# Kernel optimization log

Measured on AMD Instinct MI355X. Metric: run time of the kernel, lower is better.

The kernel has to match this reference:

```python
import jax, jax.numpy as jnp
import numpy as np

V, E, D, OUT = 100000, 400000, 128, 128
KP = 20  # kron projection dim (hard-coded 20 in module; 20*20=400)
EPS = 1e-5


def _layer_norm(x, g, b):
    mu = jnp.mean(x, axis=-1, keepdims=True)
    var = jnp.mean(jnp.square(x - mu), axis=-1, keepdims=True)
    return (x - mu) * jax.lax.rsqrt(var + EPS) * g + b


def setup_inputs() -> dict:
    key = jax.random.key(0)
    ks = jax.random.split(key, 16)
    def lin(k, fan_in, shape):
        return jax.random.normal(k, shape, jnp.float32) / np.sqrt(fan_in)
    inp = {
        'node_feats': jax.random.normal(ks[0], (V, D), jnp.float32),
        'src': jax.random.randint(ks[1], (E,), 0, V, jnp.int32),
        'dst': jax.random.randint(ks[2], (E,), 0, V, jnp.int32),
        # project_edge: Linear(2D, 1)
        'W_edge': lin(ks[3], 2 * D, (2 * D, 1)), 'b_edge': jnp.zeros((1,), jnp.float32),
        # attentive_gru.project_node: Linear(D, D)
        'W_pn': lin(ks[4], D, (D, D)), 'b_pn': jnp.zeros((D,), jnp.float32),
        # GRUCell(D, D)
        'W_ih': lin(ks[5], D, (3 * D, D)), 'b_ih': jnp.zeros((3 * D,), jnp.float32),
        'W_hh': lin(ks[6], D, (3 * D, D)), 'b_hh': jnp.zeros((3 * D,), jnp.float32),
        # layer_norm(D)
        'ln_g': jnp.ones((D,), jnp.float32), 'ln_b': jnp.zeros((D,), jnp.float32),
        # kron.proj_node: Linear(D, 20)+LN
        'Wk1': lin(ks[7], D, (D, KP)), 'bk1': jnp.zeros((KP,), jnp.float32),
        'lnk1_g': jnp.ones((KP,), jnp.float32), 'lnk1_b': jnp.zeros((KP,), jnp.float32),
        # kron.proj_kron: Linear(400, OUT)+LN
        'Wk2': lin(ks[8], KP * KP, (KP * KP, OUT)), 'bk2': jnp.zeros((OUT,), jnp.float32),
        'lnk2_g': jnp.ones((OUT,), jnp.float32), 'lnk2_b': jnp.zeros((OUT,), jnp.float32),
        # concat_proj: Linear(D+OUT, D)+LN
        'Wc': lin(ks[9], D + OUT, (D + OUT, D)), 'bc': jnp.zeros((D,), jnp.float32),
        'lnc_g': jnp.ones((D,), jnp.float32), 'lnc_b': jnp.zeros((D,), jnp.float32),
    }
    return inp


def _forward(node_feats, W_edge, b_edge, W_pn, b_pn, W_ih, b_ih, W_hh, b_hh,
             ln_g, ln_b, Wk1, bk1, lnk1_g, lnk1_b, Wk2, bk2, lnk2_g, lnk2_b,
             Wc, bc, lnc_g, lnc_b, src, dst):
    n = node_feats.shape[0]
    d = node_feats.shape[1]
    # --- Kronecker message branch ---
    npj = jax.nn.relu(_layer_norm(node_feats @ Wk1 + bk1, lnk1_g, lnk1_b))  # [V,20]
    kron = (npj[src][:, :, None] * npj[dst][:, None, :]).reshape(src.shape[0], -1)  # [E,400]
    kron = jax.nn.relu(_layer_norm(kron @ Wk2 + bk2, lnk2_g, lnk2_b))  # [E,OUT]
    kron_feat = jax.ops.segment_sum(kron, dst, num_segments=n)  # [V,OUT]
    # --- Attention branch: he = cat(dst_feats, src_feats) ---
    he = jnp.concatenate([node_feats[dst], node_feats[src]], axis=1)  # [E,2D]
    logits = jax.nn.relu(he @ W_edge + b_edge)  # [E,1]
    # edge softmax over in-edges of each dst node
    lmax = jax.ops.segment_max(logits, dst, num_segments=n)  # [V,1]
    a = jnp.exp(logits - lmax[dst])
    asum = jax.ops.segment_sum(a, dst, num_segments=n)
    a = a / asum[dst]  # [E,1]
    hv = node_feats @ W_pn + b_pn  # [V,D]
    context = jax.nn.relu(jax.ops.segment_sum(hv[src] * a, dst, num_segments=n))  # [V,D]
    # --- GRUCell(context, node_feats) ---
    gi = context @ W_ih.T + b_ih
    gh = node_feats @ W_hh.T + b_hh
    r = jax.nn.sigmoid(gi[:, :d] + gh[:, :d])
    z = jax.nn.sigmoid(gi[:, d:2 * d] + gh[:, d:2 * d])
    nn_ = jnp.tanh(gi[:, 2 * d:] + r * gh[:, 2 * d:])
    h = (1.0 - z) * nn_ + z * node_feats
    gru_out = _layer_norm(jax.nn.relu(h), ln_g, ln_b)  # [V,D]
    # --- concat + projection ---
    cat = jnp.concatenate([gru_out, kron_feat], axis=1)  # [V,D+OUT]
    return jax.nn.relu(_layer_norm(cat @ Wc + bc, lnc_g, lnc_b))


def reference(node_feats, src, dst, W_edge, b_edge, W_pn, b_pn, W_ih, b_ih, W_hh, b_hh,
              ln_g, ln_b, Wk1, bk1, lnk1_g, lnk1_b, Wk2, bk2, lnk2_g, lnk2_b,
              Wc, bc, lnc_g, lnc_b):
    return _forward(node_feats, W_edge, b_edge, W_pn, b_pn, W_ih, b_ih, W_hh, b_hh,
                    ln_g, ln_b, Wk1, bk1, lnk1_g, lnk1_b, Wk2, bk2, lnk2_g, lnk2_b,
                    Wc, bc, lnc_g, lnc_b, src, dst)
```

## Files before the change

kernel.cpp:

```cpp
#include <hip/hip_runtime.h>

#define G_KP 20
#define G_LN_EPS 1e-5f

typedef float v4f __attribute__((ext_vector_type(4)));
typedef short v8s __attribute__((ext_vector_type(8)));
typedef short v4s __attribute__((ext_vector_type(4)));

__device__ __forceinline__ unsigned short f2b(float x) {
  union { float f; unsigned int i; } c;
  c.f = x;
  return (unsigned short)((c.i + 0x7FFFu + ((c.i >> 16) & 1u)) >> 16);
}
__device__ __forceinline__ float b2f(unsigned short u) {
  union { unsigned int i; float f; } c;
  c.i = ((unsigned int)u) << 16;
  return c.f;
}

template<int NKT, int NT>
__device__ __forceinline__ void stage_mfma(
    const v8s* __restrict__ Bsrc, int kt_tiles, v8s* B_lds,
    const unsigned short* Arow, int a_kt, int a_off,
    int t, int l, v4f* acc) {
  constexpr int NPR = NT / 4;
  v8s pr[NPR];
  #pragma unroll
  for (int i = 0; i < NPR; ++i) pr[i] = Bsrc[t + i * 256];
  #pragma unroll
  for (int kt = 0; kt < NKT; ++kt) {
    __syncthreads();
    #pragma unroll
    for (int i = 0; i < NPR; ++i) B_lds[t + i * 256] = pr[i];
    if (kt + 1 < NKT) {
      #pragma unroll
      for (int i = 0; i < NPR; ++i)
        pr[i] = Bsrc[(kt + 1) * kt_tiles * 64 + t + i * 256];
    }
    __syncthreads();
    v8s a = *(const v8s*)&Arow[kt * a_kt + a_off];
    #pragma unroll
    for (int n0 = 0; n0 < NT; ++n0)
      acc[n0] = __builtin_amdgcn_mfma_f32_16x16x32_bf16(a, B_lds[n0 * 64 + l], acc[n0], 0, 0, 0);
  }
}

__global__ void GNNLayerKAFP_76871324663923_kernel() {}

__global__ void k_fill(float* out, int n, float v) {
  int i = blockIdx.x * 256 + threadIdx.x;
  if (i < n) out[i] = v;
}

__global__ void k_zero(float* p, int n) {
  int i = blockIdx.x * 256 + threadIdx.x;
  if (i < n) p[i] = 0.0f;
}

__global__ void k_prep_wk2b(const float* Wk2, unsigned short* Wk2b) {
  int id = blockIdx.x * 256 + threadIdx.x;
  if (id >= 13 * 8 * 64 * 8) return;
  int j = id & 7, l = (id >> 3) & 63, n0 = (id >> 9) & 7, kt = id >> 12;
  int k = kt * 32 + (l >> 4) * 8 + j;
  int n = n0 * 16 + (l & 15);
  Wk2b[id] = f2b((k < 400) ? Wk2[k * 128 + n] : 0.0f);
}

__global__ void k_prep_wpnb(const float* Wpn, unsigned short* WpnB) {
  int id = blockIdx.x * 256 + threadIdx.x;
  if (id >= 4 * 8 * 64 * 8) return;
  int j = id & 7, l = (id >> 3) & 63, n0 = (id >> 9) & 7, kt = id >> 12;
  int k = kt * 32 + (l >> 4) * 8 + j;
  int n = n0 * 16 + (l & 15);
  WpnB[id] = f2b(Wpn[k * 128 + n]);
}

__global__ void k_prep_wgb(const float* Wih, const float* Whh, unsigned short* WgB) {
  int id = blockIdx.x * 256 + threadIdx.x;
  if (id >= 8 * 32 * 64 * 8) return;
  int j = id & 7, l = (id >> 3) & 63, n0 = (id >> 9) & 31, kt = id >> 14;
  int k = kt * 32 + (l >> 4) * 8 + j;
  int jj = n0 * 16 + (l & 15);
  float v = 0.0f;
  if (jj < 256)      v = (k < 128) ? Wih[jj * 128 + k] : Whh[jj * 128 + (k - 128)];
  else if (jj < 384) { if (k < 128)  v = Wih[jj * 128 + k]; }
  else               { if (k >= 128) v = Whh[(jj - 128) * 128 + (k - 128)]; }
  WgB[id] = f2b(v);
}

__global__ void k_prep_wcb(const float* Wc, unsigned short* WcB) {
  int id = blockIdx.x * 256 + threadIdx.x;
  if (id >= 8 * 8 * 64 * 8) return;
  int j = id & 7, l = (id >> 3) & 63, n0 = (id >> 9) & 7, kt = id >> 12;
  int k = kt * 32 + (l >> 4) * 8 + j;
  int n = n0 * 16 + (l & 15);
  WcB[id] = f2b(Wc[k * 128 + n]);
}

__global__ void k_npj(const float* nf, const float* Wk1, const float* bk1,
                      const float* g, const float* b, float* npj) {
  int v = blockIdx.x;
  int lane = threadIdx.x;
  __shared__ float x[128];
  __shared__ float y[G_KP];
  __shared__ float st[2];
  x[lane]      = nf[v * 128 + lane];
  x[lane + 64] = nf[v * 128 + 64 + lane];
  __syncthreads();
  if (lane < G_KP) {
    float acc = bk1[lane];
    for (int t = 0; t < 128; ++t) acc += x[t] * Wk1[t * G_KP + lane];
    y[lane] = acc;
  }
  __syncthreads();
  if (lane == 0) {
    float s = 0.0f, ss = 0.0f;
    for (int i = 0; i < G_KP; ++i) { s += y[i]; ss += y[i] * y[i]; }
    float mu = s * (1.0f / G_KP);
    float var = ss * (1.0f / G_KP) - mu * mu;
    st[0] = mu;
    st[1] = rsqrtf(fmaxf(var, 0.0f) + G_LN_EPS);
  }
  __syncthreads();
  if (lane < G_KP) {
    float val = (y[lane] - st[0]) * st[1] * g[lane] + b[lane];
    npj[v * G_KP + lane] = fmaxf(val, 0.0f);
  }
}

__global__ void k_pdps(const float* nf, const float* We, float* pd, float* ps,
                       int nV) {
  int w = threadIdx.x >> 6, l = threadIdx.x & 63;
  int v = blockIdx.x * 4 + w;
  if (v >= nV) return;
  float x0 = nf[v * 128 + l], x1 = nf[v * 128 + 64 + l];
  float p0 = x0 * We[l]       + x1 * We[64 + l];
  float p1 = x0 * We[128 + l] + x1 * We[192 + l];
  for (int off = 32; off > 0; off >>= 1) {
    p0 += __shfl_down(p0, off, 64);
    p1 += __shfl_down(p1, off, 64);
  }
  if (l == 0) { pd[v] = p0; ps[v] = p1; }
}

__global__ void k_hist(const int* dst, int* deg, int nE) {
  int e = blockIdx.x * 256 + threadIdx.x;
  if (e < nE) atomicAdd(&deg[dst[e]], 1);
}

__global__ void k_scan1(const int* deg, int* bsum, int nV) {
  __shared__ int red[256];
  int b = blockIdx.x, t = threadIdx.x;
  int base = b * 2048 + t * 8;
  int s = 0;
  #pragma unroll
  for (int k = 0; k < 8; ++k) {
    int i = base + k;
    if (i < nV) s += deg[i];
  }
  red[t] = s;
  __syncthreads();
  for (int off = 128; off > 0; off >>= 1) {
    if (t < off) red[t] += red[t + off];
    __syncthreads();
  }
  if (t == 0) bsum[b] = red[0];
}

__global__ void k_scan2(const int* bsum, int* boff, int* total, int nB) {
  __shared__ int sh[1024];
  int t = threadIdx.x;
  int v = (t < nB) ? bsum[t] : 0;
  sh[t] = v;
  __syncthreads();
  for (int off = 1; off < 1024; off <<= 1) {
    int u = (t >= off) ? sh[t - off] : 0;
    __syncthreads();
    sh[t] += u;
    __syncthreads();
  }
  if (t < nB) boff[t] = sh[t] - v;
  if (t == 1023) total[0] = sh[1023];
}

__global__ void k_scan3(const int* deg, const int* boff, const int* total,
                        int* rowptr, int* cursor, int nV) {
  __shared__ int sh[256];
  int b = blockIdx.x, t = threadIdx.x;
  int base = b * 2048 + t * 8;
  int loc[8];
  int s = 0;
  #pragma unroll
  for (int k = 0; k < 8; ++k) {
    int i = base + k;
    int d = (i < nV) ? deg[i] : 0;
    loc[k] = s; s += d;
  }
  sh[t] = s;
  __syncthreads();
  for (int off = 1; off < 256; off <<= 1) {
    int u = (t >= off) ? sh[t - off] : 0;
    __syncthreads();
    sh[t] += u;
    __syncthreads();
  }
  int toff = sh[t] - s + boff[b];
  #pragma unroll
  for (int k = 0; k < 8; ++k) {
    int i = base + k;
    if (i < nV) { rowptr[i] = toff + loc[k]; cursor[i] = toff + loc[k]; }
  }
  if (b == 0 && t == 0) rowptr[nV] = total[0];
}

__global__ void k_edge(const int* src, const int* dst, const float* pd,
                       const float* ps, const float* be, float* a,
                       int* cursor, int* eid, int nE) {
  int e = blockIdx.x * 256 + threadIdx.x;
  if (e >= nE) return;
  int d = dst[e], s_ = src[e];
  float lg = fmaxf(pd[d] + ps[s_] + be[0], 0.0f);
  a[e] = __expf(fminf(lg, 60.0f));
  int pos = atomicAdd(&cursor[d], 1);
  eid[pos] = e;
}

__global__ void k_ctx_gather(const int* rowptr, const int* eid, const int* src,
                             const float* a, const float* nf, float* wctx,
                             int nV) {
  int w = threadIdx.x >> 6, l = threadIdx.x & 63;
  int v = blockIdx.x * 4 + w;
  if (v >= nV) return;
  int beg = rowptr[v], end = rowptr[v + 1];
  float s = 0.0f;
  for (int i = beg; i < end; ++i) s += a[eid[i]];
  float dn = 1.0f / fmaxf(s, 1e-20f);
  float a0 = 0.0f, a1 = 0.0f;
  for (int i = beg; i < end; ++i) {
    int e = eid[i];
    float c = a[e] * dn;
    int sn = src[e];
    a0 += c * nf[sn * 128 + l];
    a1 += c * nf[sn * 128 + 64 + l];
  }
  wctx[v * 128 + l]      = a0;
  wctx[v * 128 + 64 + l] = a1;
}

__global__ void __launch_bounds__(256, 2)
k_kron_mfma(const int* src, const int* dst, const float* npj,
            const int* rowptr, const int* eid,
            const unsigned short* Wk2b, const float* bk2,
            const float* g, const float* b, float* kf, int nE) {
  __shared__ unsigned short A_lds[64 * 424];
  __shared__ int eidx[64][2];
  __shared__ unsigned short SDB[4096];
  unsigned short (*sd)[40] = (unsigned short(*)[40])SDB;
  v8s* B_lds = (v8s*)SDB;
  float* Yf = (float*)A_lds;

  int t = threadIdx.x;
  int w = t >> 6, l = t & 63;
  int c15 = l & 15, quad = l >> 4;
  int ebase4 = w * 16;

  int ebeg = blockIdx.x * 64;
  int ecnt = nE - ebeg; if (ecnt > 64) ecnt = 64;

  if (l < 16) {
    int i = ebase4 + l;
    int e = eid[(i < ecnt) ? (ebeg + i) : ebeg];
    eidx[i][0] = src[e];
    eidx[i][1] = dst[e];
  }
  #pragma unroll
  for (int k = 0; k < 10; ++k) {
    int i = l + k * 64;
    int er = i / 40, p = i - er * 40;
    int e = ebase4 + er;
    float v = (p < 20) ? npj[eidx[e][0] * G_KP + p]
                       : npj[eidx[e][1] * G_KP + (p - 20)];
    sd[e][p] = f2b(v);
  }
  #pragma unroll
  for (int k = 0; k < 4; ++k) {
    int i = l + k * 64;
    int e = ebase4 + (i >> 4), kk = 400 + (i & 15);
    A_lds[e * 424 + kk] = 0;
  }
  #pragma unroll
  for (int k = 0; k < 5; ++k) {
    int task = l + k * 64;
    int er = task / 20;
    int i20 = task - er * 20;
    int e = ebase4 + er;
    float s = b2f(sd[e][i20]);
    int base = e * 424 + i20 * 20;
    #pragma unroll
    for (int j20 = 0; j20 < 20; ++j20)
      A_lds[base + j20] = f2b(s * b2f(sd[e][20 + j20]));
  }

  v4f acc[8];
  #pragma unroll
  for (int n0 = 0; n0 < 8; ++n0)
    #pragma unroll
    for (int r = 0; r < 4; ++r) acc[n0][r] = 0.0f;

  stage_mfma<13, 8>((const v8s*)Wk2b, 8, B_lds,
                    &A_lds[(ebase4 + c15) * 424], 32, quad * 8, t, l, acc);

  float biasv[8], gv[8], bv[8];
  #pragma unroll
  for (int n0 = 0; n0 < 8; ++n0) {
    int n = n0 * 16 + c15;
    biasv[n0] = bk2[n]; gv[n0] = g[n]; bv[n0] = b[n];
  }
  float mu[4], rs[4];
  #pragma unroll
  for (int r = 0; r < 4; ++r) {
    float s = 0.0f, q = 0.0f;
    #pragma unroll
    for (int n0 = 0; n0 < 8; ++n0) {
      float v = acc[n0][r] + biasv[n0];
      s += v; q += v * v;
    }
    for (int m = 1; m < 16; m <<= 1) {
      s += __shfl_xor(s, m, 64);
      q += __shfl_xor(q, m, 64);
    }
    float mm = s * (1.0f / 128.0f);
    float vv = q * (1.0f / 128.0f) - mm * mm;
    mu[r] = mm;
    rs[r] = rsqrtf(fmaxf(vv, 0.0f) + G_LN_EPS);
  }
  __syncthreads();
  #pragma unroll
  for (int r = 0; r < 4; ++r) {
    int eloc = ebase4 + quad * 4 + r;
    #pragma unroll
    for (int n0 = 0; n0 < 8; ++n0) {
      float v = acc[n0][r] + biasv[n0];
      Yf[eloc * 132 + n0 * 16 + c15] =
          fmaxf((v - mu[r]) * rs[r] * gv[n0] + bv[n0], 0.0f);
    }
  }
  __syncthreads();

  int dF = eidx[0][1];
  int dL = eidx[ecnt - 1][1];
  int col = t & 127;
  int wend = ebeg + ecnt;
  for (int d = dF + (t >> 7); d <= dL; d += 2) {
    int rb = rowptr[d], re = rowptr[d + 1];
    int lo = (rb > ebeg ? rb : ebeg) - ebeg;
    int hi = (re < wend ? re : wend) - ebeg;
    if (lo >= hi) continue;
    float s = 0.0f;
    for (int i = lo; i < hi; ++i) s += Yf[i * 132 + col];
    if (rb >= ebeg && re <= wend)
      kf[(size_t)d * 128 + col] = s;
    else
      atomicAdd(&kf[(size_t)d * 128 + col], s);
  }
}

__global__ void __launch_bounds__(256, 2)
k_gru_mfma(const float* nf, const float* wctx, const float* kf,
           const unsigned short* WpnB, const float* bpn,
           const unsigned short* WgB,
           const float* b_ih, const float* b_hh,
           const float* g1, const float* b1,
           const unsigned short* WcB, const float* bc,
           const float* g2, const float* b2, float* out,
           int nV) {
  __shared__ unsigned short CX[64][264];
  __shared__ v8s B_lds[1024];
  int t = threadIdx.x;
  int w = t >> 6, l = t & 63;
  int c15 = l & 15, quad = l >> 4;
  int v0 = blockIdx.x * 64;
  int rowbase = w * 16;

  #pragma unroll
  for (int k = 0; k < 8; ++k) {
    int i = l + k * 64;
    int r = i >> 5;
    int seg = i & 31;
    int vn = v0 + rowbase + r; if (vn >= nV) vn = nV - 1;
    v4f wc = *(const v4f*)&wctx[vn * 128 + seg * 4];
    v4f xf = *(const v4f*)&nf[vn * 128 + seg * 4];
    v4s pw = { (short)f2b(wc[0]), (short)f2b(wc[1]), (short)f2b(wc[2]), (short)f2b(wc[3]) };
    v4s px = { (short)f2b(xf[0]), (short)f2b(xf[1]), (short)f2b(xf[2]), (short)f2b(xf[3]) };
    *(v4s*)&CX[rowbase + r][seg * 4]       = pw;
    *(v4s*)&CX[rowbase + r][128 + seg * 4] = px;
  }

  {
    v4f acc[8];
    #pragma unroll
    for (int n0 = 0; n0 < 8; ++n0)
      #pragma unroll
      for (int r = 0; r < 4; ++r) acc[n0][r] = 0.0f;
    stage_mfma<4, 8>((const v8s*)WpnB, 8, B_lds,
                     &CX[rowbase + c15][0], 32, quad * 8, t, l, acc);
    #pragma unroll
    for (int n0 = 0; n0 < 8; ++n0) {
      int n = n0 * 16 + c15;
      float bo = bpn[n];
      #pragma unroll
      for (int r = 0; r < 4; ++r)
        CX[rowbase + quad * 4 + r][n] = f2b(fmaxf(acc[n0][r] + bo, 0.0f));
    }
  }

  unsigned int rz[32];
  {
    v4f acc[16];
    #pragma unroll
    for (int n0 = 0; n0 < 16; ++n0)
      #pragma unroll
      for (int r = 0; r < 4; ++r) acc[n0][r] = 0.0f;
    stage_mfma<8, 16>((const v8s*)WgB, 32, B_lds,
                      &CX[rowbase + c15][0], 32, quad * 8, t, l, acc);
    #pragma unroll
    for (int n0 = 0; n0 < 8; ++n0) {
      int j = n0 * 16 + c15;
      float brz = b_ih[j] + b_hh[j];
      float bzz = b_ih[128 + j] + b_hh[128 + j];
      #pragma unroll
      for (int r = 0; r < 4; ++r) {
        float rp = acc[n0][r] + brz;
        float zp = acc[8 + n0][r] + bzz;
        float rr = 1.0f / (1.0f + __expf(-fmaxf(fminf(rp, 30.0f), -30.0f)));
        float zz = 1.0f / (1.0f + __expf(-fmaxf(fminf(zp, 30.0f), -30.0f)));
        rz[r * 8 + n0] = (unsigned int)f2b(rr) | ((unsigned int)f2b(zz) << 16);
      }
    }
  }
  {
    v4f acc[16];
    #pragma unroll
    for (int n0 = 0; n0 < 16; ++n0)
      #pragma unroll
      for (int r = 0; r < 4; ++r) acc[n0][r] = 0.0f;
    stage_mfma<8, 16>((const v8s*)WgB + 16 * 64, 32, B_lds,
                      &CX[rowbase + c15][0], 32, quad * 8, t, l, acc);
    #pragma unroll
    for (int r = 0; r < 4; ++r) {
      int row = rowbase + quad * 4 + r;
      float h[8];
      float s = 0.0f, q = 0.0f;
      #pragma unroll
      for (int n0 = 0; n0 < 8; ++n0) {
        int j = n0 * 16 + c15;
        float gi = acc[n0][r] + b_ih[256 + j];
        float gh = acc[8 + n0][r] + b_hh[256 + j];
        unsigned int pk = rz[r * 8 + n0];
        float rr = b2f((unsigned short)(pk & 0xFFFFu));
        float zz = b2f((unsigned short)(pk >> 16));
        float an = fmaxf(fminf(gi + rr * gh, 15.0f), -15.0f);
        float e2 = __expf(-2.0f * an);
        float nn = (1.0f - e2) / (1.0f + e2);
        float x  = b2f(CX[row][128 + j]);
        float hv = fmaxf((1.0f - zz) * nn + zz * x, 0.0f);
        h[n0] = hv; s += hv; q += hv * hv;
      }
      for (int m = 1; m < 16; m <<= 1) {
        s += __shfl_xor(s, m, 64);
        q += __shfl_xor(q, m, 64);
      }
      float mu = s * (1.0f / 128.0f);
      float var = q * (1.0f / 128.0f) - mu * mu;
      float rstd = rsqrtf(fmaxf(var, 0.0f) + G_LN_EPS);
      #pragma unroll
      for (int n0 = 0; n0 < 8; ++n0) {
        int j = n0 * 16 + c15;
        CX[row][j] = f2b((h[n0] - mu) * rstd * g1[j] + b1[j]);
      }
    }
  }

  #pragma unroll
  for (int k = 0; k < 8; ++k) {
    int i = l + k * 64;
    int r = i >> 5, seg = i & 31;
    int vn = v0 + rowbase + r; if (vn >= nV) vn = nV - 1;
    v4f kv = *(const v4f*)&kf[vn * 128 + seg * 4];
    v4s pk = { (short)f2b(kv[0]), (short)f2b(kv[1]), (short)f2b(kv[2]), (short)f2b(kv[3]) };
    *(v4s*)&CX[rowbase + r][128 + seg * 4] = pk;
  }

  {
    v4f acc[8];
    #pragma unroll
    for (int n0 = 0; n0 < 8; ++n0)
      #pragma unroll
      for (int r = 0; r < 4; ++r) acc[n0][r] = 0.0f;
    stage_mfma<8, 8>((const v8s*)WcB, 8, B_lds,
                     &CX[rowbase + c15][0], 32, quad * 8, t, l, acc);
    #pragma unroll
    for (int r = 0; r < 4; ++r) {
      float vv[8];
      float s = 0.0f, q = 0.0f;
      #pragma unroll
      for (int n0 = 0; n0 < 8; ++n0) {
        vv[n0] = acc[n0][r] + bc[n0 * 16 + c15];
        s += vv[n0]; q += vv[n0] * vv[n0];
      }
      for (int m = 1; m < 16; m <<= 1) {
        s += __shfl_xor(s, m, 64);
        q += __shfl_xor(q, m, 64);
      }
      float mu = s * (1.0f / 128.0f);
      float var = q * (1.0f / 128.0f) - mu * mu;
      float rstd = rsqrtf(fmaxf(var, 0.0f) + G_LN_EPS);
      int vn = v0 + rowbase + quad * 4 + r;
      if (vn < nV) {
        #pragma unroll
        for (int n0 = 0; n0 < 8; ++n0) {
          int n = n0 * 16 + c15;
          float y = fmaxf((vv[n0] - mu) * rstd * g2[n] + b2[n], 0.0f);
          if (y != y) y = 9.0f;
          out[vn * 128 + n] = y;
        }
      }
    }
  }
}

extern "C" void kernel_launch(void* const* d_in, const int* in_sizes, int n_in,
                              void* d_out, int out_size, void* d_ws, size_t ws_size,
                              hipStream_t stream) {
  (void)n_in;

  int nV = in_sizes[0] / 128;
  int nE = in_sizes[1];

  const float* nf     = (const float*)d_in[0];
  const int*   src    = (const int*)d_in[1];
  const int*   dst    = (const int*)d_in[2];
  const float* W_edge = (const float*)d_in[3];
  const float* b_edge = (const float*)d_in[4];
  const float* W_pn   = (const float*)d_in[5];
  const float* b_pn   = (const float*)d_in[6];
  const float* W_ih   = (const float*)d_in[7];
  const float* b_ih   = (const float*)d_in[8];
  const float* W_hh   = (const float*)d_in[9];
  const float* b_hh   = (const float*)d_in[10];
  const float* ln_g   = (const float*)d_in[11];
  const float* ln_b   = (const float*)d_in[12];
  const float* Wk1    = (const float*)d_in[13];
  const float* bk1    = (const float*)d_in[14];
  const float* lnk1_g = (const float*)d_in[15];
  const float* lnk1_b = (const float*)d_in[16];
  const float* Wk2    = (const float*)d_in[17];
  const float* bk2    = (const float*)d_in[18];
  const float* lnk2_g = (const float*)d_in[19];
  const float* lnk2_b = (const float*)d_in[20];
  const float* Wc     = (const float*)d_in[21];
  const float* bc     = (const float*)d_in[22];
  const float* lnc_g  = (const float*)d_in[23];
  const float* lnc_b  = (const float*)d_in[24];

  float* ws = (float*)d_ws;
  size_t off = 0;
  float* w_npj  = ws + off; off += (size_t)nV * G_KP;
  float* w_a    = ws + off; off += (size_t)nE;
  float* w_pd   = ws + off; off += (size_t)nV;
  float* w_ps   = ws + off; off += (size_t)nV;
  int*   w_rowp = (int*)(ws + off); off += (size_t)nV + 1;
  int*   w_curs = (int*)(ws + off); off += (size_t)nV;
  int*   w_eid  = (int*)(ws + off); off += (size_t)nE;
  int*   w_bsum = (int*)(ws + off); off += 1024;
  int*   w_boff = (int*)(ws + off); off += 1024;
  int*   w_tot  = (int*)(ws + off); off += 1;
  float* w_wctx = ws + off; off += (size_t)nV * 128;
  int*   w_deg  = (int*)(ws + off); off += (size_t)nV;
  float* w_kf   = ws + off; off += (size_t)nV * 128;
  unsigned short* w_wk2b = (unsigned short*)(ws + off); off += 26624;
  unsigned short* w_wpnb = (unsigned short*)(ws + off); off += 8192;
  unsigned short* w_wgb  = (unsigned short*)(ws + off); off += 65536;
  unsigned short* w_wcb  = (unsigned short*)(ws + off); off += 16384;
  size_t need_bytes = off * 4;

  if (ws_size < need_bytes) {
    k_fill<<<(out_size + 255) / 256, 256, 0, stream>>>((float*)d_out, out_size, 7.0f);
    return;
  }

  k_fill<<<(out_size + 255) / 256, 256, 0, stream>>>((float*)d_out, out_size, 2.0f);

  int nzero = nV * 129;
  k_zero<<<(nzero + 255) / 256, 256, 0, stream>>>((float*)w_deg, nzero);
  k_prep_wk2b<<<208, 256, 0, stream>>>(Wk2, w_wk2b);
  k_prep_wpnb<<<64, 256, 0, stream>>>(W_pn, w_wpnb);
  k_prep_wgb<<<512, 256, 0, stream>>>(W_ih, W_hh, w_wgb);
  k_prep_wcb<<<128, 256, 0, stream>>>(Wc, w_wcb);

  int nB = (nV + 2047) / 2048;
  k_npj<<<nV, 64, 0, stream>>>(nf, Wk1, bk1, lnk1_g, lnk1_b, w_npj);
  k_pdps<<<(nV + 3) / 4, 256, 0, stream>>>(nf, W_edge, w_pd, w_ps, nV);
  k_hist<<<(nE + 255) / 256, 256, 0, stream>>>(dst, w_deg, nE);
  k_scan1<<<nB, 256, 0, stream>>>(w_deg, w_bsum, nV);
  k_scan2<<<1, 1024, 0, stream>>>(w_bsum, w_boff, w_tot, nB);
  k_scan3<<<nB, 256, 0, stream>>>(w_deg, w_boff, w_tot, w_rowp, w_curs, nV);
  k_edge<<<(nE + 255) / 256, 256, 0, stream>>>(src, dst, w_pd, w_ps, b_edge,
                                               w_a, w_curs, w_eid, nE);
  k_ctx_gather<<<(nV + 3) / 4, 256, 0, stream>>>(w_rowp, w_eid, src, w_a, nf,
                                                 w_wctx, nV);
  k_kron_mfma<<<(nE + 63) / 64, 256, 0, stream>>>(src, dst, w_npj, w_rowp,
                                                  w_eid, w_wk2b, bk2,
                                                  lnk2_g, lnk2_b, w_kf, nE);
  k_gru_mfma<<<(nV + 63) / 64, 256, 0, stream>>>(nf, w_wctx, w_kf, w_wpnb, b_pn,
                                                 w_wgb, b_ih, b_hh, ln_g, ln_b,
                                                 w_wcb, bc, lnc_g, lnc_b,
                                                 (float*)d_out, nV);
}
```

Before: 770.1 us.

## Split kron MFMA work across wave pairs with 32-edge blocks

The kron kernel now handles 32 edges per block instead of 64. Each pair of waves shares a 16-edge row tile, and each wave computes half of the 128 output columns. LayerNorm statistics are combined across the two halves through a small shared-memory exchange, and launch bounds are raised to allow more resident blocks. The aim is less LDS and fewer registers per block for higher occupancy, at the cost of twice as many blocks, extra barriers, and more reloading of the B weights and boundary segment-sum work.

```diff
diff --git a/kernel.cpp b/kernel.cpp
--- a/kernel.cpp
+++ b/kernel.cpp
@@ -18,12 +18,12 @@
   return c.f;
 }
 
-template<int NKT, int NT>
-__device__ __forceinline__ void stage_mfma(
+template<int NKT, int NTS, int NTU>
+__device__ __forceinline__ void stage_mfma2(
     const v8s* __restrict__ Bsrc, int kt_tiles, v8s* B_lds,
-    const unsigned short* Arow, int a_kt, int a_off,
+    const unsigned short* Arow, int a_kt, int a_off, int b_off,
     int t, int l, v4f* acc) {
-  constexpr int NPR = NT / 4;
+  constexpr int NPR = NTS / 4;
   v8s pr[NPR];
   #pragma unroll
   for (int i = 0; i < NPR; ++i) pr[i] = Bsrc[t + i * 256];
@@ -40,8 +40,8 @@
     __syncthreads();
     v8s a = *(const v8s*)&Arow[kt * a_kt + a_off];
     #pragma unroll
-    for (int n0 = 0; n0 < NT; ++n0)
-      acc[n0] = __builtin_amdgcn_mfma_f32_16x16x32_bf16(a, B_lds[n0 * 64 + l], acc[n0], 0, 0, 0);
+    for (int n0 = 0; n0 < NTU; ++n0)
+      acc[n0] = __builtin_amdgcn_mfma_f32_16x16x32_bf16(a, B_lds[b_off + n0 * 64 + l], acc[n0], 0, 0, 0);
   }
 }
 
@@ -247,14 +247,15 @@
   wctx[v * 128 + 64 + l] = a1;
 }
 
-__global__ void __launch_bounds__(256, 2)
+__global__ void __launch_bounds__(256, 4)
 k_kron_mfma(const int* src, const int* dst, const float* npj,
             const int* rowptr, const int* eid,
             const unsigned short* Wk2b, const float* bk2,
             const float* g, const float* b, float* kf, int nE) {
-  __shared__ unsigned short A_lds[64 * 424];
-  __shared__ int eidx[64][2];
+  __shared__ unsigned short A_lds[32 * 424];
+  __shared__ int eidx[32][2];
   __shared__ unsigned short SDB[4096];
+  __shared__ float psq[2][2][16][2];
   unsigned short (*sd)[40] = (unsigned short(*)[40])SDB;
   v8s* B_lds = (v8s*)SDB;
   float* Yf = (float*)A_lds;
@@ -262,66 +263,60 @@
   int t = threadIdx.x;
   int w = t >> 6, l = t & 63;
   int c15 = l & 15, quad = l >> 4;
-  int ebase4 = w * 16;
-
-  int ebeg = blockIdx.x * 64;
-  int ecnt = nE - ebeg; if (ecnt > 64) ecnt = 64;
-
-  if (l < 16) {
-    int i = ebase4 + l;
-    int e = eid[(i < ecnt) ? (ebeg + i) : ebeg];
-    eidx[i][0] = src[e];
-    eidx[i][1] = dst[e];
-  }
-  #pragma unroll
-  for (int k = 0; k < 10; ++k) {
-    int i = l + k * 64;
+  int pg = w >> 1, hf = w & 1;
+  int erbase = pg * 16;
+
+  int ebeg = blockIdx.x * 32;
+  int ecnt = nE - ebeg; if (ecnt > 32) ecnt = 32;
+
+  if (t < 32) {
+    int e = eid[(t < ecnt) ? (ebeg + t) : ebeg];
+    eidx[t][0] = src[e];
+    eidx[t][1] = dst[e];
+  }
+  __syncthreads();
+  for (int i = t; i < 1280; i += 256) {
     int er = i / 40, p = i - er * 40;
-    int e = ebase4 + er;
-    float v = (p < 20) ? npj[eidx[e][0] * G_KP + p]
-                       : npj[eidx[e][1] * G_KP + (p - 20)];
-    sd[e][p] = f2b(v);
-  }
-  #pragma unroll
-  for (int k = 0; k < 4; ++k) {
-    int i = l + k * 64;
-    int e = ebase4 + (i >> 4), kk = 400 + (i & 15);
+    float v = (p < 20) ? npj[eidx[er][0] * G_KP + p]
+                       : npj[eidx[er][1] * G_KP + (p - 20)];
+    sd[er][p] = f2b(v);
+  }
+  __syncthreads();
+  for (int i = t; i < 32 * 16; i += 256) {
+    int e = i >> 4, kk = 400 + (i & 15);
     A_lds[e * 424 + kk] = 0;
   }
-  #pragma unroll
-  for (int k = 0; k < 5; ++k) {
-    int task = l + k * 64;
-    int er = task / 20;
-    int i20 = task - er * 20;
-    int e = ebase4 + er;
-    float s = b2f(sd[e][i20]);
-    int base = e * 424 + i20 * 20;
+  for (int task = t; task < 640; task += 256) {
+    int er = task / 20, i20 = task - er * 20;
+    float s = b2f(sd[er][i20]);
+    int base = er * 424 + i20 * 20;
     #pragma unroll
     for (int j20 = 0; j20 < 20; ++j20)
-      A_lds[base + j20] = f2b(s * b2f(sd[e][20 + j20]));
-  }
-
-  v4f acc[8];
-  #pragma unroll
-  for (int n0 = 0; n0 < 8; ++n0)
+      A_lds[base + j20] = f2b(s * b2f(sd[er][20 + j20]));
+  }
+
+  v4f acc[4];
+  #pragma unroll
+  for (int n0 = 0; n0 < 4; ++n0)
     #pragma unroll
     for (int r = 0; r < 4; ++r) acc[n0][r] = 0.0f;
 
-  stage_mfma<13, 8>((const v8s*)Wk2b, 8, B_lds,
-                    &A_lds[(ebase4 + c15) * 424], 32, quad * 8, t, l, acc);
-
-  float biasv[8], gv[8], bv[8];
-  #pragma unroll
-  for (int n0 = 0; n0 < 8; ++n0) {
-    int n = n0 * 16 + c15;
+  stage_mfma2<13, 8, 4>((const v8s*)Wk2b, 8, B_lds,
+                        &A_lds[(erbase + c15) * 424], 32, quad * 8,
+                        hf * 256, t, l, acc);
+
+  float biasv[4], gv[4], bv[4];
+  #pragma unroll
+  for (int n0 = 0; n0 < 4; ++n0) {
+    int n = hf * 64 + n0 * 16 + c15;
     biasv[n0] = bk2[n]; gv[n0] = g[n]; bv[n0] = b[n];
   }
-  float mu[4], rs[4];
+  float sArr[4], qArr[4];
   #pragma unroll
   for (int r = 0; r < 4; ++r) {
     float s = 0.0f, q = 0.0f;
     #pragma unroll
-    for (int n0 = 0; n0 < 8; ++n0) {
+    for (int n0 = 0; n0 < 4; ++n0) {
       float v = acc[n0][r] + biasv[n0];
       s += v; q += v * v;
     }
@@ -329,19 +324,30 @@
       s += __shfl_xor(s, m, 64);
       q += __shfl_xor(q, m, 64);
     }
+    sArr[r] = s; qArr[r] = q;
+    if (c15 == 0) {
+      psq[pg][hf][quad * 4 + r][0] = s;
+      psq[pg][hf][quad * 4 + r][1] = q;
+    }
+  }
+  __syncthreads();
+  float mu[4], rs[4];
+  #pragma unroll
+  for (int r = 0; r < 4; ++r) {
+    float s = sArr[r] + psq[pg][hf ^ 1][quad * 4 + r][0];
+    float q = qArr[r] + psq[pg][hf ^ 1][quad * 4 + r][1];
     float mm = s * (1.0f / 128.0f);
     float vv = q * (1.0f / 128.0f) - mm * mm;
     mu[r] = mm;
     rs[r] = rsqrtf(fmaxf(vv, 0.0f) + G_LN_EPS);
   }
-  __syncthreads();
   #pragma unroll
   for (int r = 0; r < 4; ++r) {
-    int eloc = ebase4 + quad * 4 + r;
-    #pragma unroll
-    for (int n0 = 0; n0 < 8; ++n0) {
+    int eloc = erbase + quad * 4 + r;
+    #pragma unroll
+    for (int n0 = 0; n0 < 4; ++n0) {
       float v = acc[n0][r] + biasv[n0];
-      Yf[eloc * 132 + n0 * 16 + c15] =
+      Yf[eloc * 132 + hf * 64 + n0 * 16 + c15] =
           fmaxf((v - mu[r]) * rs[r] * gv[n0] + bv[n0], 0.0f);
     }
   }
@@ -402,8 +408,8 @@
     for (int n0 = 0; n0 < 8; ++n0)
       #pragma unroll
       for (int r = 0; r < 4; ++r) acc[n0][r] = 0.0f;
-    stage_mfma<4, 8>((const v8s*)WpnB, 8, B_lds,
-                     &CX[rowbase + c15][0], 32, quad * 8, t, l, acc);
+    stage_mfma2<4, 8, 8>((const v8s*)WpnB, 8, B_lds,
+                         &CX[rowbase + c15][0], 32, quad * 8, 0, t, l, acc);
     #pragma unroll
     for (int n0 = 0; n0 < 8; ++n0) {
       int n = n0 * 16 + c15;
@@ -421,8 +427,8 @@
     for (int n0 = 0; n0 < 16; ++n0)
       #pragma unroll
       for (int r = 0; r < 4; ++r) acc[n0][r] = 0.0f;
-    stage_mfma<8, 16>((const v8s*)WgB, 32, B_lds,
-                      &CX[rowbase + c15][0], 32, quad * 8, t, l, acc);
+    stage_mfma2<8, 16, 16>((const v8s*)WgB, 32, B_lds,
+                           &CX[rowbase + c15][0], 32, quad * 8, 0, t, l, acc);
     #pragma unroll
     for (int n0 = 0; n0 < 8; ++n0) {
       int j = n0 * 16 + c15;
@@ -444,8 +450,8 @@
     for (int n0 = 0; n0 < 16; ++n0)
       #pragma unroll
       for (int r = 0; r < 4; ++r) acc[n0][r] = 0.0f;
-    stage_mfma<8, 16>((const v8s*)WgB + 16 * 64, 32, B_lds,
-                      &CX[rowbase + c15][0], 32, quad * 8, t, l, acc);
+    stage_mfma2<8, 16, 16>((const v8s*)WgB + 16 * 64, 32, B_lds,
+                           &CX[rowbase + c15][0], 32, quad * 8, 0, t, l, acc);
     #pragma unroll
     for (int r = 0; r < 4; ++r) {
       int row = rowbase + quad * 4 + r;
@@ -497,8 +503,8 @@
     for (int n0 = 0; n0 < 8; ++n0)
       #pragma unroll
       for (int r = 0; r < 4; ++r) acc[n0][r] = 0.0f;
-    stage_mfma<8, 8>((const v8s*)WcB, 8, B_lds,
-                     &CX[rowbase + c15][0], 32, quad * 8, t, l, acc);
+    stage_mfma2<8, 8, 8>((const v8s*)WcB, 8, B_lds,
+                         &CX[rowbase + c15][0], 32, quad * 8, 0, t, l, acc);
     #pragma unroll
     for (int r = 0; r < 4; ++r) {
       float vv[8];
@@ -609,7 +615,7 @@
                                                w_a, w_curs, w_eid, nE);
   k_ctx_gather<<<(nV + 3) / 4, 256, 0, stream>>>(w_rowp, w_eid, src, w_a, nf,
                                                  w_wctx, nV);
-  k_kron_mfma<<<(nE + 63) / 64, 256, 0, stream>>>(src, dst, w_npj, w_rowp,
+  k_kron_mfma<<<(nE + 31) / 32, 256, 0, stream>>>(src, dst, w_npj, w_rowp,
                                                   w_eid, w_wk2b, bk2,
                                                   lnk2_g, lnk2_b, w_kf, nE);
   k_gru_mfma<<<(nV + 63) / 64, 256, 0, stream>>>(nf, w_wctx, w_kf, w_wpnb, b_pn,
```

Measured after the change: 741.4 us. -3.7%, faster.
